# Kernel optimization log

Measured on AMD Instinct MI355X. Metric: run time of the kernel, lower is better.

Reference implementation:

```python
import jax, jax.numpy as jnp
import numpy as np

DIM = 1024
H = 16
D = DIM // H  # head_dim = 64
SCALE = D ** (-0.5)


def _gate_mlp(x, w1, b1, w2, b2):
    # Linear -> ReLU -> Linear -> Sigmoid
    h = jax.nn.relu(x @ w1 + b1)
    return jax.nn.sigmoid(h @ w2 + b2)


def _heads(t, B, N):
    # [B,N,C] -> [B,H,N,D]
    return t.reshape(B, N, H, D).transpose(0, 2, 1, 3)


def setup_inputs() -> dict:
    key = jax.random.key(0)
    ks = jax.random.split(key, 12)
    s = 1.0 / np.sqrt(DIM)
    inp = {
        "x1": jax.random.normal(ks[0], (4, 4096, DIM), jnp.float32),
        "x2": jax.random.normal(ks[1], (4, 4096, DIM), jnp.float32),
        # kv projections (no bias, qkv_bias=False); stored as [in, out]
        "Wkv1": jax.random.normal(ks[2], (DIM, 2 * DIM), jnp.float32) * s,
        "Wkv2": jax.random.normal(ks[3], (DIM, 2 * DIM), jnp.float32) * s,
        # gate MLP 1
        "g1_w1": jax.random.normal(ks[4], (DIM, DIM), jnp.float32) * s,
        "g1_b1": jnp.zeros((DIM,), jnp.float32),
        "g1_w2": jax.random.normal(ks[5], (DIM, DIM), jnp.float32) * s,
        "g1_b2": jnp.zeros((DIM,), jnp.float32),
        # gate MLP 2
        "g2_w1": jax.random.normal(ks[6], (DIM, DIM), jnp.float32) * s,
        "g2_b1": jnp.zeros((DIM,), jnp.float32),
        "g2_w2": jax.random.normal(ks[7], (DIM, DIM), jnp.float32) * s,
        "g2_b2": jnp.zeros((DIM,), jnp.float32),
    }
    return inp


def reference(x1, x2, Wkv1, Wkv2, g1_w1, g1_b1, g1_w2, g1_b2, g2_w1, g2_b1, g2_w2, g2_b2):
    B, N, C = x1.shape

    q1 = _heads(x1, B, N)  # [B,H,N,D]
    q2 = _heads(x2, B, N)

    kv1 = (x1 @ Wkv1).reshape(B, N, 2, H, D).transpose(2, 0, 3, 1, 4)
    k1, v1 = kv1[0], kv1[1]  # [B,H,N,D]
    kv2 = (x2 @ Wkv2).reshape(B, N, 2, H, D).transpose(2, 0, 3, 1, 4)
    k2, v2 = kv2[0], kv2[1]

    gate1 = _heads(_gate_mlp(x1, g1_w1, g1_b1, g1_w2, g1_b2), B, N)
    gate2 = _heads(_gate_mlp(x2, g2_w1, g2_b1, g2_w2, g2_b2), B, N)

    # context: k^T @ (v*gate) -> [B,H,D,D], softmax over first D axis (dim=-2)
    ctx1 = jnp.einsum('bhnd,bhne->bhde', k1, v1 * gate1) * SCALE
    ctx1 = jax.nn.softmax(ctx1, axis=-2)
    ctx2 = jnp.einsum('bhnd,bhne->bhde', k2, v2 * gate2) * SCALE
    ctx2 = jax.nn.softmax(ctx2, axis=-2)

    # cross: x1 attends via ctx2, x2 via ctx1
    o1 = jnp.einsum('bhnd,bhde->bhne', q1, ctx2).transpose(0, 2, 1, 3).reshape(B, N, C)
    o2 = jnp.einsum('bhnd,bhde->bhne', q2, ctx1).transpose(0, 2, 1, 3).reshape(B, N, C)
    return (o1, o2)
```

## Files before the change

### kernel.cpp

```cpp
#include <hip/hip_runtime.h>
#include <hip/hip_bf16.h>

typedef __attribute__((ext_vector_type(8))) short bf16x8_t;
typedef __attribute__((ext_vector_type(4))) float f32x4_t;
typedef unsigned short u16;
typedef unsigned int u32;

#define GLL16(gp, lp) \
    __builtin_amdgcn_global_load_lds((const __attribute__((address_space(1))) u32*)(gp), \
                                     (__attribute__((address_space(3))) u32*)(lp), 16, 0, 0)

__device__ __forceinline__ float bf2f(unsigned int u16v) {
    union { unsigned int i; float f; } c;
    c.i = (u16v & 0xffffu) << 16;
    return c.f;
}
__device__ __forceinline__ unsigned short f2bf(float f) {
    union { float f; unsigned int i; } c; c.f = f;
    unsigned int x = c.i;
    unsigned int r = (x + 0x7fffu + ((x >> 16) & 1u)) >> 16;
    return (unsigned short)r;
}


__global__ void cast_x_kernel(const float* __restrict__ in, u16* __restrict__ hi, int n4) {
    int i = blockIdx.x * blockDim.x + threadIdx.x;
    int stride = gridDim.x * blockDim.x;
    for (; i < n4; i += stride) {
        float4 v = *(const float4*)(in + (size_t)i * 4);
        ushort4 h;
        h.x = f2bf(v.x); h.y = f2bf(v.y); h.z = f2bf(v.z); h.w = f2bf(v.w);
        *(ushort4*)(hi + (size_t)i * 4) = h;
    }
}

__global__ __launch_bounds__(256) void cast_wt_kernel(const float* __restrict__ W,
                                                      u16* __restrict__ Wt,
                                                      int K, int N) {
    __shared__ u16 tile[32][33];
    int c0 = blockIdx.x * 32, k0 = blockIdx.y * 32;
    int tx = threadIdx.x & 31, ty = threadIdx.x >> 5;
#pragma unroll
    for (int i = 0; i < 4; ++i) {
        int k = k0 + ty + i * 8;
        tile[ty + i * 8][tx] = f2bf(W[(size_t)k * N + c0 + tx]);
    }
    __syncthreads();
#pragma unroll
    for (int i = 0; i < 4; ++i) {
        int c = c0 + ty + i * 8;
        Wt[(size_t)c * K + k0 + tx] = tile[tx][ty + i * 8];
    }
}

__global__ __launch_bounds__(256) void cast_wt_split_kernel(const float* __restrict__ W,
                                                            u16* __restrict__ Wh,
                                                            u16* __restrict__ Wl,
                                                            int K, int N) {
    __shared__ u16 th[32][33];
    __shared__ u16 tl[32][33];
    int c0 = blockIdx.x * 32, k0 = blockIdx.y * 32;
    int tx = threadIdx.x & 31, ty = threadIdx.x >> 5;
#pragma unroll
    for (int i = 0; i < 4; ++i) {
        int k = k0 + ty + i * 8;
        float f = W[(size_t)k * N + c0 + tx];
        unsigned short h = f2bf(f);
        th[ty + i * 8][tx] = h;
        tl[ty + i * 8][tx] = f2bf(f - bf2f(h));
    }
    __syncthreads();
#pragma unroll
    for (int i = 0; i < 4; ++i) {
        int c = c0 + ty + i * 8;
        Wh[(size_t)c * K + k0 + tx] = th[tx][ty + i * 8];
        Wl[(size_t)c * K + k0 + tx] = tl[tx][ty + i * 8];
    }
}


__device__ __forceinline__ void stage32(u16* lds_buf, const u16* __restrict__ gbase, int tid) {
#pragma unroll
    for (int g = 0; g < 2; ++g) {
        int c = tid + g * 256;
        int row = c >> 2, qp = c & 3;
        int qs = qp ^ ((row >> 1) & 3);
        GLL16(gbase + (size_t)row * 1024 + qs * 8, lds_buf + c * 8);
    }
}

template <int EPI>
__global__ __launch_bounds__(256, 4) void gemm128_kernel(
    const u16* __restrict__ Ah,
    const u16* __restrict__ Bh, const u16* __restrict__ Bl,
    const float* __restrict__ bias,
    u16* __restrict__ out_bf, float* __restrict__ out_f,
    float* __restrict__ gate_vg, float* __restrict__ kout,
    int N)
{
    __shared__ u16 As[128 * 32];
    __shared__ u16 Bs[128 * 32];
    const int NT = (EPI == 2) ? 64 : 32;

    int nwg = 128 * (N >> 7);
    int wg = blockIdx.y * 128 + blockIdx.x;
    int cpx = nwg >> 3;
    wg = (wg & 7) * cpx + (wg >> 3);
    int bx = wg & 127, by = wg >> 7;
    int row0 = bx << 7, col0 = by << 7;

    const int tid = threadIdx.x;
    const int lane = tid & 63;
    const int w = tid >> 6;
    const int wm = w >> 1, wn = w & 1;
    const int fr = lane & 15, fq = lane >> 4;

    auto abase = [&](int kt) -> const u16* {
        if (EPI == 2) return Ah + (size_t)row0 * 1024 + (kt >> 1) * 32;
        return Ah + (size_t)row0 * 1024 + kt * 32;
    };
    auto bbase = [&](int kt) -> const u16* {
        if (EPI == 2) return ((kt & 1) ? Bl : Bh) + (size_t)col0 * 1024 + (kt >> 1) * 32;
        return Bh + (size_t)col0 * 1024 + kt * 32;
    };

    f32x4_t acc[4][4];
#pragma unroll
    for (int m = 0; m < 4; ++m)
#pragma unroll
        for (int n = 0; n < 4; ++n) acc[m][n] = (f32x4_t)(0.0f);

    const int slot = (fq ^ ((fr >> 1) & 3)) * 8;
    int aoff[4], boff[4];
#pragma unroll
    for (int m = 0; m < 4; ++m) aoff[m] = (wm * 64 + m * 16 + fr) * 32 + slot;
#pragma unroll
    for (int n = 0; n < 4; ++n) boff[n] = (wn * 64 + n * 16 + fr) * 32 + slot;

    for (int kt = 0; kt < NT; ++kt) {
        if (EPI != 2 || (kt & 1) == 0)
            stage32(As, abase(kt), tid);
        stage32(Bs, bbase(kt), tid);
        __syncthreads();

        bf16x8_t a[4], b[4];
#pragma unroll
        for (int m = 0; m < 4; ++m) a[m] = *(const bf16x8_t*)&As[aoff[m]];
#pragma unroll
        for (int n = 0; n < 4; ++n) b[n] = *(const bf16x8_t*)&Bs[boff[n]];
#pragma unroll
        for (int m = 0; m < 4; ++m)
#pragma unroll
            for (int n = 0; n < 4; ++n)
                acc[m][n] = __builtin_amdgcn_mfma_f32_16x16x32_bf16(a[m], b[n], acc[m][n], 0, 0, 0);
        __syncthreads();
    }

#pragma unroll
    for (int m = 0; m < 4; ++m) {
        int row = row0 + wm * 64 + m * 16 + fq * 4;
#pragma unroll
        for (int n = 0; n < 4; ++n) {
            int col = col0 + wn * 64 + n * 16 + fr;
            if (EPI == 0) {
                float bv = bias[col];
#pragma unroll
                for (int rr = 0; rr < 4; ++rr)
                    out_bf[(size_t)(row + rr) * N + col] = f2bf(fmaxf(acc[m][n][rr] + bv, 0.0f));
            } else if (EPI == 1) {
                float bv = bias[col];
#pragma unroll
                for (int rr = 0; rr < 4; ++rr)
                    out_f[(size_t)(row + rr) * N + col] = 1.0f / (1.0f + __expf(-(acc[m][n][rr] + bv)));
            } else {
                if (col < 1024) {
#pragma unroll
                    for (int rr = 0; rr < 4; ++rr)
                        kout[(size_t)(row + rr) * 1024 + col] = acc[m][n][rr];
                } else {
#pragma unroll
                    for (int rr = 0; rr < 4; ++rr) {
                        size_t idx = (size_t)(row + rr) * 1024 + (col - 1024);
                        gate_vg[idx] = acc[m][n][rr] * gate_vg[idx];
                    }
                }
            }
        }
    }
}

__global__ __launch_bounds__(256) void ctx_part_kernel(
    const float* __restrict__ kmat,
    const float* __restrict__ vmat,
    float* __restrict__ part)
{
    int bh = blockIdx.x & 63;
    int p  = blockIdx.x >> 6;
    int b = bh >> 4, h = bh & 15;
    int n0 = p * 512;
    __shared__ float ks[128][64];
    __shared__ float vs[128][64];
    int t = threadIdx.x;
    int dg = t & 15, eg = t >> 4;
    float acc[4][4];
#pragma unroll
    for (int i = 0; i < 4; ++i)
#pragma unroll
        for (int j = 0; j < 4; ++j) acc[i][j] = 0.0f;

    const float* kb = kmat + (size_t)b * 4096 * 1024 + h * 64;
    const float* vb = vmat + (size_t)b * 4096 * 1024 + h * 64;

    for (int c0 = 0; c0 < 512; c0 += 128) {
        __syncthreads();
#pragma unroll
        for (int s = 0; s < 8; ++s) {
            int ci = t + s * 256;
            int r = ci >> 4, o4 = (ci & 15) * 4;
            size_t g = (size_t)(n0 + c0 + r) * 1024 + o4;
            *(float4*)(&ks[r][o4]) = *(const float4*)(kb + g);
            *(float4*)(&vs[r][o4]) = *(const float4*)(vb + g);
        }
        __syncthreads();
#pragma unroll 4
        for (int n = 0; n < 128; ++n) {
            float4 k4 = *(const float4*)(&ks[n][dg * 4]);
            float4 v4 = *(const float4*)(&vs[n][eg * 4]);
            acc[0][0] += k4.x * v4.x; acc[0][1] += k4.x * v4.y; acc[0][2] += k4.x * v4.z; acc[0][3] += k4.x * v4.w;
            acc[1][0] += k4.y * v4.x; acc[1][1] += k4.y * v4.y; acc[1][2] += k4.y * v4.z; acc[1][3] += k4.y * v4.w;
            acc[2][0] += k4.z * v4.x; acc[2][1] += k4.z * v4.y; acc[2][2] += k4.z * v4.z; acc[2][3] += k4.z * v4.w;
            acc[3][0] += k4.w * v4.x; acc[3][1] += k4.w * v4.y; acc[3][2] += k4.w * v4.z; acc[3][3] += k4.w * v4.w;
        }
    }
    float* pp = part + ((size_t)(p * 64 + bh)) * 64 * 64;
#pragma unroll
    for (int i = 0; i < 4; ++i)
#pragma unroll
        for (int j = 0; j < 4; ++j)
            pp[(dg * 4 + i) * 64 + (eg * 4 + j)] = acc[i][j];
}

__global__ __launch_bounds__(256) void softmax_ctx_kernel(const float* __restrict__ part,
                                                          float* __restrict__ ctx) {
    int bh = blockIdx.x;
    int t = threadIdx.x;
    int e = t & 63, dq = t >> 6;
    __shared__ float red[4][68];
    float loc[16];
    float m = -1e30f;
#pragma unroll
    for (int i = 0; i < 16; ++i) {
        int d = dq * 16 + i;
        float s = 0.f;
#pragma unroll
        for (int p = 0; p < 8; ++p)
            s += part[(((size_t)(p * 64 + bh)) * 64 + d) * 64 + e];
        s *= 0.125f;
        loc[i] = s;
        m = fmaxf(m, s);
    }
    red[dq][e] = m;
    __syncthreads();
    float M = fmaxf(fmaxf(red[0][e], red[1][e]), fmaxf(red[2][e], red[3][e]));
    float sum = 0.f;
#pragma unroll
    for (int i = 0; i < 16; ++i) {
        float v = __expf(loc[i] - M);
        loc[i] = v;
        sum += v;
    }
    __syncthreads();
    red[dq][e] = sum;
    __syncthreads();
    float inv = 1.0f / (red[0][e] + red[1][e] + red[2][e] + red[3][e]);
#pragma unroll
    for (int i = 0; i < 16; ++i) {
        int d = dq * 16 + i;
        ctx[((size_t)bh * 64 + d) * 64 + e] = loc[i] * inv;
    }
}

__global__ __launch_bounds__(256) void out_gemm_kernel(
    const float* __restrict__ x, const float* __restrict__ ctx, float* __restrict__ out)
{
    int id = blockIdx.x;
    int nc = id & 63;
    int h = (id >> 6) & 15;
    int b = id >> 10;
    size_t r0 = (size_t)b * 4096 + nc * 64;
    __shared__ float xs[64][65];
    __shared__ float cs[64][64];
    int t = threadIdx.x;
    for (int idx = t; idx < 4096; idx += 256) {
        int rr = idx >> 6, d = idx & 63;
        xs[rr][d] = x[(r0 + rr) * 1024 + h * 64 + d];
    }
    const float* cb = ctx + ((size_t)(b * 16 + h)) * 4096;
    for (int idx = t; idx < 4096; idx += 256) {
        cs[idx >> 6][idx & 63] = cb[idx];
    }
    __syncthreads();
    int eg = t & 15, nl = t >> 4;
    for (int rr = nl; rr < 64; rr += 16) {
        float a0 = 0.f, a1 = 0.f, a2 = 0.f, a3 = 0.f;
#pragma unroll
        for (int d = 0; d < 64; ++d) {
            float xv = xs[rr][d];
            float4 cv = *(const float4*)(&cs[d][eg * 4]);
            a0 += xv * cv.x; a1 += xv * cv.y; a2 += xv * cv.z; a3 += xv * cv.w;
        }
        float4 o = make_float4(a0, a1, a2, a3);
        *(float4*)(&out[(r0 + rr) * 1024 + h * 64 + eg * 4]) = o;
    }
}


extern "C" void kernel_launch(void* const* d_in, const int* in_sizes, int n_in,
                              void* d_out, int out_size, void* d_ws, size_t ws_size,
                              hipStream_t stream)
{
    (void)in_sizes; (void)n_in; (void)out_size; (void)ws_size;
    const float* x1   = (const float*)d_in[0];
    const float* x2   = (const float*)d_in[1];
    const float* Wkv1 = (const float*)d_in[2];
    const float* Wkv2 = (const float*)d_in[3];
    const float* g1w1 = (const float*)d_in[4];
    const float* g1b1 = (const float*)d_in[5];
    const float* g1w2 = (const float*)d_in[6];
    const float* g1b2 = (const float*)d_in[7];
    const float* g2w1 = (const float*)d_in[8];
    const float* g2b1 = (const float*)d_in[9];
    const float* g2w2 = (const float*)d_in[10];
    const float* g2b2 = (const float*)d_in[11];
    float* out = (float*)d_out;

    char* ws = (char*)d_ws;
    size_t off = 0;
    auto alloc = [&](size_t b) { void* p = ws + off; off += (b + 255) & ~(size_t)255; return p; };
    const size_t NTOK = 16384;
    u16* xh    = (u16*)alloc(NTOK * 1024 * 2);
    u16* wkv1h = (u16*)alloc((size_t)2048 * 1024 * 2);
    u16* wkv1l = (u16*)alloc((size_t)2048 * 1024 * 2);
    u16* wkv2h = (u16*)alloc((size_t)2048 * 1024 * 2);
    u16* wkv2l = (u16*)alloc((size_t)2048 * 1024 * 2);
    u16* g1w1t = (u16*)alloc((size_t)1024 * 1024 * 2);
    u16* g1w2t = (u16*)alloc((size_t)1024 * 1024 * 2);
    u16* g2w1t = (u16*)alloc((size_t)1024 * 1024 * 2);
    u16* g2w2t = (u16*)alloc((size_t)1024 * 1024 * 2);
    u16* hbuf  = (u16*)alloc(NTOK * 1024 * 2);
    float* gate = (float*)alloc(NTOK * 1024 * 4);
    float* kbuf = (float*)alloc(NTOK * 1024 * 4);
    float* part = (float*)alloc((size_t)8 * 64 * 64 * 64 * 4);
    float* ctx1 = (float*)alloc((size_t)64 * 64 * 64 * 4);
    float* ctx2 = (float*)alloc((size_t)64 * 64 * 64 * 4);

    cast_wt_split_kernel<<<dim3(64, 32), 256, 0, stream>>>(Wkv1, wkv1h, wkv1l, 1024, 2048);
    cast_wt_split_kernel<<<dim3(64, 32), 256, 0, stream>>>(Wkv2, wkv2h, wkv2l, 1024, 2048);
    cast_wt_kernel<<<dim3(32, 32), 256, 0, stream>>>(g1w1, g1w1t, 1024, 1024);
    cast_wt_kernel<<<dim3(32, 32), 256, 0, stream>>>(g1w2, g1w2t, 1024, 1024);
    cast_wt_kernel<<<dim3(32, 32), 256, 0, stream>>>(g2w1, g2w1t, 1024, 1024);
    cast_wt_kernel<<<dim3(32, 32), 256, 0, stream>>>(g2w2, g2w2t, 1024, 1024);

    cast_x_kernel<<<2048, 256, 0, stream>>>(x1, xh, (int)(NTOK * 1024 / 4));
    gemm128_kernel<0><<<dim3(128, 8), 256, 0, stream>>>(xh, g1w1t, nullptr, g1b1,
                                                        hbuf, nullptr, nullptr, nullptr, 1024);
    gemm128_kernel<1><<<dim3(128, 8), 256, 0, stream>>>(hbuf, g1w2t, nullptr, g1b2,
                                                        nullptr, gate, nullptr, nullptr, 1024);
    gemm128_kernel<2><<<dim3(128, 16), 256, 0, stream>>>(xh, wkv1h, wkv1l, nullptr,
                                                         nullptr, nullptr, gate, kbuf, 2048);
    ctx_part_kernel<<<512, 256, 0, stream>>>(kbuf, gate, part);
    softmax_ctx_kernel<<<64, 256, 0, stream>>>(part, ctx1);

    cast_x_kernel<<<2048, 256, 0, stream>>>(x2, xh, (int)(NTOK * 1024 / 4));
    gemm128_kernel<0><<<dim3(128, 8), 256, 0, stream>>>(xh, g2w1t, nullptr, g2b1,
                                                        hbuf, nullptr, nullptr, nullptr, 1024);
    gemm128_kernel<1><<<dim3(128, 8), 256, 0, stream>>>(hbuf, g2w2t, nullptr, g2b2,
                                                        nullptr, gate, nullptr, nullptr, 1024);
    gemm128_kernel<2><<<dim3(128, 16), 256, 0, stream>>>(xh, wkv2h, wkv2l, nullptr,
                                                         nullptr, nullptr, gate, kbuf, 2048);
    ctx_part_kernel<<<512, 256, 0, stream>>>(kbuf, gate, part);
    softmax_ctx_kernel<<<64, 256, 0, stream>>>(part, ctx2);

    out_gemm_kernel<<<4096, 256, 0, stream>>>(x1, ctx2, out);
    out_gemm_kernel<<<4096, 256, 0, stream>>>(x2, ctx1, out + 16777216);
}
```

Baseline: 927.2 us.

## Double-buffer GEMM LDS tiles and merge per-input cast and output launches

The bf16 GEMM kernel now keeps two LDS buffers for each of A and B. It prefetches the next K-slice while MFMAs run on the current one, which removes one barrier per iteration. In the split-weight variant, each A slice is loaded once per pair of K steps. The weight casts, input casts and both output GEMMs are each merged into single launches using blockIdx.z or a block-id split, and x1 and x2 get separate bf16 buffers. This doubles LDS use per block, which may limit occupancy, and adds a second 32 MB workspace buffer.

```diff
diff --git a/kernel.cpp b/kernel.cpp
--- a/kernel.cpp
+++ b/kernel.cpp
@@ -23,20 +23,29 @@
 }
 
 
-__global__ void cast_x_kernel(const float* __restrict__ in, u16* __restrict__ hi, int n4) {
+__global__ void cast_x2_kernel(const float* __restrict__ x1, const float* __restrict__ x2,
+                               u16* __restrict__ h1, u16* __restrict__ h2, int n4) {
     int i = blockIdx.x * blockDim.x + threadIdx.x;
     int stride = gridDim.x * blockDim.x;
     for (; i < n4; i += stride) {
-        float4 v = *(const float4*)(in + (size_t)i * 4);
+        float4 v = *(const float4*)(x1 + (size_t)i * 4);
         ushort4 h;
         h.x = f2bf(v.x); h.y = f2bf(v.y); h.z = f2bf(v.z); h.w = f2bf(v.w);
-        *(ushort4*)(hi + (size_t)i * 4) = h;
-    }
-}
-
-__global__ __launch_bounds__(256) void cast_wt_kernel(const float* __restrict__ W,
-                                                      u16* __restrict__ Wt,
-                                                      int K, int N) {
+        *(ushort4*)(h1 + (size_t)i * 4) = h;
+        v = *(const float4*)(x2 + (size_t)i * 4);
+        h.x = f2bf(v.x); h.y = f2bf(v.y); h.z = f2bf(v.z); h.w = f2bf(v.w);
+        *(ushort4*)(h2 + (size_t)i * 4) = h;
+    }
+}
+
+__global__ __launch_bounds__(256) void cast_wt4_kernel(
+    const float* __restrict__ W0, const float* __restrict__ W1,
+    const float* __restrict__ W2, const float* __restrict__ W3,
+    u16* __restrict__ T0, u16* __restrict__ T1,
+    u16* __restrict__ T2, u16* __restrict__ T3,
+    int K, int N) {
+    const float* W = (blockIdx.z == 0) ? W0 : (blockIdx.z == 1) ? W1 : (blockIdx.z == 2) ? W2 : W3;
+    u16* Wt = (blockIdx.z == 0) ? T0 : (blockIdx.z == 1) ? T1 : (blockIdx.z == 2) ? T2 : T3;
     __shared__ u16 tile[32][33];
     int c0 = blockIdx.x * 32, k0 = blockIdx.y * 32;
     int tx = threadIdx.x & 31, ty = threadIdx.x >> 5;
@@ -53,10 +62,14 @@
     }
 }
 
-__global__ __launch_bounds__(256) void cast_wt_split_kernel(const float* __restrict__ W,
-                                                            u16* __restrict__ Wh,
-                                                            u16* __restrict__ Wl,
-                                                            int K, int N) {
+__global__ __launch_bounds__(256) void cast_wt_split2_kernel(
+    const float* __restrict__ W0, const float* __restrict__ W1,
+    u16* __restrict__ H0, u16* __restrict__ L0,
+    u16* __restrict__ H1, u16* __restrict__ L1,
+    int K, int N) {
+    const float* W = blockIdx.z ? W1 : W0;
+    u16* Wh = blockIdx.z ? H1 : H0;
+    u16* Wl = blockIdx.z ? L1 : L0;
     __shared__ u16 th[32][33];
     __shared__ u16 tl[32][33];
     int c0 = blockIdx.x * 32, k0 = blockIdx.y * 32;
@@ -98,8 +111,8 @@
     float* __restrict__ gate_vg, float* __restrict__ kout,
     int N)
 {
-    __shared__ u16 As[128 * 32];
-    __shared__ u16 Bs[128 * 32];
+    __shared__ u16 As[2][4096];
+    __shared__ u16 Bs[2][4096];
     const int NT = (EPI == 2) ? 64 : 32;
 
     int nwg = 128 * (N >> 7);
@@ -115,10 +128,8 @@
     const int wm = w >> 1, wn = w & 1;
     const int fr = lane & 15, fq = lane >> 4;
 
-    auto abase = [&](int kt) -> const u16* {
-        if (EPI == 2) return Ah + (size_t)row0 * 1024 + (kt >> 1) * 32;
-        return Ah + (size_t)row0 * 1024 + kt * 32;
-    };
+    const u16* Ab0 = Ah + (size_t)row0 * 1024;
+    auto aslice = [&](int s) { return Ab0 + s * 32; };
     auto bbase = [&](int kt) -> const u16* {
         if (EPI == 2) return ((kt & 1) ? Bl : Bh) + (size_t)col0 * 1024 + (kt >> 1) * 32;
         return Bh + (size_t)col0 * 1024 + kt * 32;
@@ -137,23 +148,35 @@
 #pragma unroll
     for (int n = 0; n < 4; ++n) boff[n] = (wn * 64 + n * 16 + fr) * 32 + slot;
 
+    stage32(As[0], aslice(0), tid);
+    stage32(Bs[0], bbase(0), tid);
+
     for (int kt = 0; kt < NT; ++kt) {
-        if (EPI != 2 || (kt & 1) == 0)
-            stage32(As, abase(kt), tid);
-        stage32(Bs, bbase(kt), tid);
         __syncthreads();
 
+        if (kt + 1 < NT) {
+            stage32(Bs[(kt + 1) & 1], bbase(kt + 1), tid);
+            if (EPI == 2) {
+                int s1 = (kt >> 1) + 1;
+                if ((kt & 1) == 0 && s1 < 32)
+                    stage32(As[s1 & 1], aslice(s1), tid);
+            } else {
+                stage32(As[(kt + 1) & 1], aslice(kt + 1), tid);
+            }
+        }
+
+        const int ab = (EPI == 2) ? ((kt >> 1) & 1) : (kt & 1);
+        const int bb = kt & 1;
         bf16x8_t a[4], b[4];
 #pragma unroll
-        for (int m = 0; m < 4; ++m) a[m] = *(const bf16x8_t*)&As[aoff[m]];
-#pragma unroll
-        for (int n = 0; n < 4; ++n) b[n] = *(const bf16x8_t*)&Bs[boff[n]];
+        for (int m = 0; m < 4; ++m) a[m] = *(const bf16x8_t*)&As[ab][aoff[m]];
+#pragma unroll
+        for (int n = 0; n < 4; ++n) b[n] = *(const bf16x8_t*)&Bs[bb][boff[n]];
 #pragma unroll
         for (int m = 0; m < 4; ++m)
 #pragma unroll
             for (int n = 0; n < 4; ++n)
                 acc[m][n] = __builtin_amdgcn_mfma_f32_16x16x32_bf16(a[m], b[n], acc[m][n], 0, 0, 0);
-        __syncthreads();
     }
 
 #pragma unroll
@@ -281,12 +304,20 @@
 }
 
 __global__ __launch_bounds__(256) void out_gemm_kernel(
-    const float* __restrict__ x, const float* __restrict__ ctx, float* __restrict__ out)
+    const float* __restrict__ x1, const float* __restrict__ x2,
+    const float* __restrict__ ctxA,
+    const float* __restrict__ ctxB,
+    float* __restrict__ out)
 {
     int id = blockIdx.x;
-    int nc = id & 63;
-    int h = (id >> 6) & 15;
-    int b = id >> 10;
+    int s = id >> 12;
+    int r = id & 4095;
+    int nc = r & 63;
+    int h = (r >> 6) & 15;
+    int b = r >> 10;
+    const float* x = s ? x2 : x1;
+    const float* ctx = s ? ctxB : ctxA;
+    float* o = out + (size_t)s * 16777216;
     size_t r0 = (size_t)b * 4096 + nc * 64;
     __shared__ float xs[64][65];
     __shared__ float cs[64][64];
@@ -309,8 +340,8 @@
             float4 cv = *(const float4*)(&cs[d][eg * 4]);
             a0 += xv * cv.x; a1 += xv * cv.y; a2 += xv * cv.z; a3 += xv * cv.w;
         }
-        float4 o = make_float4(a0, a1, a2, a3);
-        *(float4*)(&out[(r0 + rr) * 1024 + h * 64 + eg * 4]) = o;
+        float4 ov = make_float4(a0, a1, a2, a3);
+        *(float4*)(&o[(r0 + rr) * 1024 + h * 64 + eg * 4]) = ov;
     }
 }
 
@@ -338,7 +369,8 @@
     size_t off = 0;
     auto alloc = [&](size_t b) { void* p = ws + off; off += (b + 255) & ~(size_t)255; return p; };
     const size_t NTOK = 16384;
-    u16* xh    = (u16*)alloc(NTOK * 1024 * 2);
+    u16* xh1   = (u16*)alloc(NTOK * 1024 * 2);
+    u16* xh2   = (u16*)alloc(NTOK * 1024 * 2);
     u16* wkv1h = (u16*)alloc((size_t)2048 * 1024 * 2);
     u16* wkv1l = (u16*)alloc((size_t)2048 * 1024 * 2);
     u16* wkv2h = (u16*)alloc((size_t)2048 * 1024 * 2);
@@ -354,33 +386,29 @@
     float* ctx1 = (float*)alloc((size_t)64 * 64 * 64 * 4);
     float* ctx2 = (float*)alloc((size_t)64 * 64 * 64 * 4);
 
-    cast_wt_split_kernel<<<dim3(64, 32), 256, 0, stream>>>(Wkv1, wkv1h, wkv1l, 1024, 2048);
-    cast_wt_split_kernel<<<dim3(64, 32), 256, 0, stream>>>(Wkv2, wkv2h, wkv2l, 1024, 2048);
-    cast_wt_kernel<<<dim3(32, 32), 256, 0, stream>>>(g1w1, g1w1t, 1024, 1024);
-    cast_wt_kernel<<<dim3(32, 32), 256, 0, stream>>>(g1w2, g1w2t, 1024, 1024);
-    cast_wt_kernel<<<dim3(32, 32), 256, 0, stream>>>(g2w1, g2w1t, 1024, 1024);
-    cast_wt_kernel<<<dim3(32, 32), 256, 0, stream>>>(g2w2, g2w2t, 1024, 1024);
-
-    cast_x_kernel<<<2048, 256, 0, stream>>>(x1, xh, (int)(NTOK * 1024 / 4));
-    gemm128_kernel<0><<<dim3(128, 8), 256, 0, stream>>>(xh, g1w1t, nullptr, g1b1,
+    cast_wt_split2_kernel<<<dim3(64, 32, 2), 256, 0, stream>>>(Wkv1, Wkv2,
+                                                               wkv1h, wkv1l, wkv2h, wkv2l, 1024, 2048);
+    cast_wt4_kernel<<<dim3(32, 32, 4), 256, 0, stream>>>(g1w1, g1w2, g2w1, g2w2,
+                                                         g1w1t, g1w2t, g2w1t, g2w2t, 1024, 1024);
+    cast_x2_kernel<<<2048, 256, 0, stream>>>(x1, x2, xh1, xh2, (int)(NTOK * 1024 / 4));
+
+    gemm128_kernel<0><<<dim3(128, 8), 256, 0, stream>>>(xh1, g1w1t, nullptr, g1b1,
                                                         hbuf, nullptr, nullptr, nullptr, 1024);
     gemm128_kernel<1><<<dim3(128, 8), 256, 0, stream>>>(hbuf, g1w2t, nullptr, g1b2,
                                                         nullptr, gate, nullptr, nullptr, 1024);
-    gemm128_kernel<2><<<dim3(128, 16), 256, 0, stream>>>(xh, wkv1h, wkv1l, nullptr,
+    gemm128_kernel<2><<<dim3(128, 16), 256, 0, stream>>>(xh1, wkv1h, wkv1l, nullptr,
                                                          nullptr, nullptr, gate, kbuf, 2048);
     ctx_part_kernel<<<512, 256, 0, stream>>>(kbuf, gate, part);
     softmax_ctx_kernel<<<64, 256, 0, stream>>>(part, ctx1);
 
-    cast_x_kernel<<<2048, 256, 0, stream>>>(x2, xh, (int)(NTOK * 1024 / 4));
-    gemm128_kernel<0><<<dim3(128, 8), 256, 0, stream>>>(xh, g2w1t, nullptr, g2b1,
+    gemm128_kernel<0><<<dim3(128, 8), 256, 0, stream>>>(xh2, g2w1t, nullptr, g2b1,
                                                         hbuf, nullptr, nullptr, nullptr, 1024);
     gemm128_kernel<1><<<dim3(128, 8), 256, 0, stream>>>(hbuf, g2w2t, nullptr, g2b2,
                                                         nullptr, gate, nullptr, nullptr, 1024);
-    gemm128_kernel<2><<<dim3(128, 16), 256, 0, stream>>>(xh, wkv2h, wkv2l, nullptr,
+    gemm128_kernel<2><<<dim3(128, 16), 256, 0, stream>>>(xh2, wkv2h, wkv2l, nullptr,
                                                          nullptr, nullptr, gate, kbuf, 2048);
     ctx_part_kernel<<<512, 256, 0, stream>>>(kbuf, gate, part);
     softmax_ctx_kernel<<<64, 256, 0, stream>>>(part, ctx2);
 
-    out_gemm_kernel<<<4096, 256, 0, stream>>>(x1, ctx2, out);
-    out_gemm_kernel<<<4096, 256, 0, stream>>>(x2, ctx1, out + 16777216);
-}
+    out_gemm_kernel<<<8192, 256, 0, stream>>>(x1, x2, ctx2, ctx1, out);
+}
```

Result: no change. 932.0 us (+0.5%).
